# Kernel optimization log

Measured on AMD Instinct MI355X. Metric: run time of the kernel, lower is better.

The kernel has to match this reference:

```python
import jax, jax.numpy as jnp
import numpy as np

NUM_EXPERTS = 8
TOP_K = 2
AUX_COEF = 0.01
B, S, D, H = 4, 2048, 1024, 684


def setup_inputs() -> dict:
    key = jax.random.key(0)
    ks = jax.random.split(key, 5)
    scale_d = 1.0 / np.sqrt(D)
    scale_h = 1.0 / np.sqrt(H)
    return {
        "x": jax.random.normal(ks[0], (B, S, D), dtype=jnp.float32),
        "router_w": jax.random.normal(ks[1], (NUM_EXPERTS, D), dtype=jnp.float32) * scale_d,
        "w1": jax.random.normal(ks[2], (NUM_EXPERTS, H, D), dtype=jnp.float32) * scale_d,
        "w2": jax.random.normal(ks[3], (NUM_EXPERTS, D, H), dtype=jnp.float32) * scale_h,
        "w3": jax.random.normal(ks[4], (NUM_EXPERTS, H, D), dtype=jnp.float32) * scale_d,
    }


def reference(x, router_w, w1, w2, w3):
    b, s, d = x.shape
    xf = x.reshape(-1, d)                                   # [T, d]
    probs = jax.nn.softmax(xf @ router_w.T, axis=-1)        # [T, E]
    topk_probs, topk_idx = jax.lax.top_k(probs, TOP_K)      # [T, k]

    # aux load-balancing loss (uses top-1 assignment density)
    density = jnp.mean(jax.nn.one_hot(topk_idx[:, 0], NUM_EXPERTS, dtype=xf.dtype), axis=0)
    aux_loss = AUX_COEF * jnp.sum(density * probs.mean(axis=0)) * NUM_EXPERTS

    # per-token per-expert combine weight (sums probs if an expert repeats across slots)
    combine = jnp.sum(jax.nn.one_hot(topk_idx, NUM_EXPERTS, dtype=xf.dtype)
                      * topk_probs[..., None], axis=1)      # [T, E]

    out = jnp.zeros_like(xf)
    for e in range(NUM_EXPERTS):  # fixed small expert loop
        h = jax.nn.silu(xf @ w1[e].T) * (xf @ w3[e].T)      # [T, H] SwiGLU
        out = out + combine[:, e:e + 1] * (h @ w2[e].T)     # weighted scatter-combine
    return out.reshape(b, s, d), aux_loss
```

## Files before the change

### kernel.cpp

```cpp
#include <hip/hip_runtime.h>
#include <hip/hip_bf16.h>

#define T_TOK 8192
#define DMODEL 1024
#define HDIM 684
#define HPAD 704
#define NEXP 8

typedef short  bf16x8  __attribute__((ext_vector_type(8)));
typedef float  f32x4   __attribute__((ext_vector_type(4)));

__device__ inline unsigned short f2bu(float f) {
    __hip_bfloat16 h = __float2bfloat16(f);
    return *reinterpret_cast<unsigned short*>(&h);
}

typedef const __attribute__((address_space(1))) unsigned int* gas_p;
typedef __attribute__((address_space(3))) unsigned int* las_p;
__device__ inline void ld_lds16(const unsigned short* g, unsigned short* l) {
    __builtin_amdgcn_global_load_lds((gas_p)g, (las_p)l, 16, 0, 0);
}


__global__ __launch_bounds__(256) void cvt_all(
    const float* __restrict__ w1, const float* __restrict__ w3, const float* __restrict__ w2,
    unsigned short* __restrict__ w1b, unsigned short* __restrict__ w3b,
    unsigned short* __restrict__ w2b, int n4, int n2)
{
    int i = blockIdx.x * 256 + threadIdx.x;
    if (i < 2 * n4) {
        const float* src; unsigned short* dst; int j;
        if (i < n4) { src = w1; dst = w1b; j = i; }
        else        { src = w3; dst = w3b; j = i - n4; }
        float4 v = ((const float4*)src)[j];
        ((ushort4*)dst)[j] = make_ushort4(f2bu(v.x), f2bu(v.y), f2bu(v.z), f2bu(v.w));
        return;
    }
    int j = i - 2 * n4;
    if (j >= n2) return;
    int row = j / 176;
    int col = (j - row * 176) * 4;
    ushort4 o = make_ushort4(0, 0, 0, 0);
    if (col < HDIM) {
        float4 v = *(const float4*)(w2 + (size_t)row * HDIM + col);
        o = make_ushort4(f2bu(v.x), f2bu(v.y), f2bu(v.z), f2bu(v.w));
    }
    *(ushort4*)(w2b + (size_t)row * HPAD + col) = o;
}

__global__ __launch_bounds__(256) void moe_router(
    const float* __restrict__ x, const float* __restrict__ rw,
    unsigned short* __restrict__ xb,
    float* __restrict__ blk_psum, int* __restrict__ blk_t1, int* __restrict__ blk_pc,
    int* __restrict__ topk_idx, float* __restrict__ topk_p)
{
    __shared__ float sp[4][NEXP];
    __shared__ int   si1[4], si2[4];

    int lane = threadIdx.x & 63;
    int w    = threadIdx.x >> 6;
    int t    = blockIdx.x * 4 + w;
    const float* xr = x + (size_t)t * DMODEL;
    unsigned short* xbr = xb + (size_t)t * DMODEL;

    float acc[NEXP];
#pragma unroll
    for (int e = 0; e < NEXP; ++e) acc[e] = 0.f;
#pragma unroll
    for (int j = 0; j < DMODEL / 64; ++j) {
        float xv = xr[j * 64 + lane];
        xbr[j * 64 + lane] = f2bu(xv);
#pragma unroll
        for (int e = 0; e < NEXP; ++e)
            acc[e] += xv * rw[e * DMODEL + j * 64 + lane];
    }
#pragma unroll
    for (int off = 32; off > 0; off >>= 1) {
#pragma unroll
        for (int e = 0; e < NEXP; ++e)
            acc[e] += __shfl_xor(acc[e], off, 64);
    }
    if (lane == 0) {
        float m = acc[0];
#pragma unroll
        for (int e = 1; e < NEXP; ++e) m = fmaxf(m, acc[e]);
        float p[NEXP]; float s = 0.f;
#pragma unroll
        for (int e = 0; e < NEXP; ++e) { p[e] = expf(acc[e] - m); s += p[e]; }
        float inv = 1.f / s;
#pragma unroll
        for (int e = 0; e < NEXP; ++e) p[e] *= inv;
        int i1 = 0;
#pragma unroll
        for (int e = 1; e < NEXP; ++e) if (p[e] > p[i1]) i1 = e;
        int i2 = (i1 == 0) ? 1 : 0;
#pragma unroll
        for (int e = 0; e < NEXP; ++e) if (e != i1 && p[e] > p[i2]) i2 = e;

        topk_idx[t * 2 + 0] = i1;  topk_idx[t * 2 + 1] = i2;
        topk_p[t * 2 + 0] = p[i1]; topk_p[t * 2 + 1] = p[i2];
#pragma unroll
        for (int e = 0; e < NEXP; ++e) sp[w][e] = p[e];
        si1[w] = i1; si2[w] = i2;
    }
    __syncthreads();
    if (threadIdx.x < NEXP) {
        int e = threadIdx.x;
        float ps = sp[0][e] + sp[1][e] + sp[2][e] + sp[3][e];
        int t1 = (si1[0] == e) + (si1[1] == e) + (si1[2] == e) + (si1[3] == e);
        int pc = t1 + (si2[0] == e) + (si2[1] == e) + (si2[2] == e) + (si2[3] == e);
        blk_psum[blockIdx.x * NEXP + e] = ps;
        blk_t1[blockIdx.x * NEXP + e]  = t1;
        blk_pc[blockIdx.x * NEXP + e]  = pc;
    }
}

__global__ __launch_bounds__(256) void moe_scan(
    const float* __restrict__ blk_psum, const int* __restrict__ blk_t1,
    const int* __restrict__ blk_pc,
    int* pair_count, int* offsets, int* cursor, float* aux_out)
{
    __shared__ float wp[4][NEXP];
    __shared__ int   wt[4][NEXP], wc[4][NEXP];
    __shared__ float tp[NEXP];
    __shared__ int   tt1[NEXP], tpc[NEXP];

    int tid = threadIdx.x;
    int lane = tid & 63, w = tid >> 6;
    float lp[NEXP]; int lt[NEXP], lc[NEXP];
#pragma unroll
    for (int e = 0; e < NEXP; ++e) { lp[e] = 0.f; lt[e] = 0; lc[e] = 0; }
    for (int b = tid; b < 2048; b += 256)
#pragma unroll
        for (int e = 0; e < NEXP; ++e) {
            lp[e] += blk_psum[b * NEXP + e];
            lt[e] += blk_t1[b * NEXP + e];
            lc[e] += blk_pc[b * NEXP + e];
        }
#pragma unroll
    for (int off = 32; off > 0; off >>= 1) {
#pragma unroll
        for (int e = 0; e < NEXP; ++e) {
            lp[e] += __shfl_xor(lp[e], off, 64);
            lt[e] += __shfl_xor(lt[e], off, 64);
            lc[e] += __shfl_xor(lc[e], off, 64);
        }
    }
    if (lane == 0) {
#pragma unroll
        for (int e = 0; e < NEXP; ++e) { wp[w][e] = lp[e]; wt[w][e] = lt[e]; wc[w][e] = lc[e]; }
    }
    __syncthreads();
    if (tid < NEXP) {
        int e = tid;
        float s = wp[0][e] + wp[1][e] + wp[2][e] + wp[3][e];
        int t1 = wt[0][e] + wt[1][e] + wt[2][e] + wt[3][e];
        int pc = wc[0][e] + wc[1][e] + wc[2][e] + wc[3][e];
        tp[e] = s; tt1[e] = t1; tpc[e] = pc;
        pair_count[e] = pc;
    }
    __syncthreads();
    if (tid == 0) {
        int run = 0;
        for (int e = 0; e < NEXP; ++e) { offsets[e] = run; cursor[e] = run; run += tpc[e]; }
        float s = 0.f;
        for (int e = 0; e < NEXP; ++e)
            s += ((float)tt1[e] / (float)T_TOK) * (tp[e] / (float)T_TOK);
        aux_out[0] = 0.01f * s * (float)NEXP;
    }
}

__global__ __launch_bounds__(256) void moe_scatter(
    const int* __restrict__ topk_idx, const float* __restrict__ topk_p,
    int* cursor, int* __restrict__ pair_token, float* __restrict__ pair_prob)
{
    __shared__ int lcnt[NEXP], gbase[NEXP];
    int tid = threadIdx.x;
    if (tid < NEXP) lcnt[tid] = 0;
    __syncthreads();
    int t = blockIdx.x * 256 + tid;
    int e0 = topk_idx[t * 2 + 0], e1 = topk_idx[t * 2 + 1];
    int p0 = atomicAdd(&lcnt[e0], 1);
    int p1 = atomicAdd(&lcnt[e1], 1);
    __syncthreads();
    if (tid < NEXP) gbase[tid] = atomicAdd(&cursor[tid], lcnt[tid]);
    __syncthreads();
    int q0 = gbase[e0] + p0, q1 = gbase[e1] + p1;
    pair_token[q0] = t; pair_prob[q0] = topk_p[t * 2 + 0];
    pair_token[q1] = t; pair_prob[q1] = topk_p[t * 2 + 1];
}


__global__ __launch_bounds__(512, 4) void moe_ffn1(
    const unsigned short* __restrict__ xb, const unsigned short* __restrict__ w1b,
    const unsigned short* __restrict__ w3b,
    const int* __restrict__ pair_count, const int* __restrict__ offsets,
    const int* __restrict__ pair_token,
    unsigned short* __restrict__ h)
{
    int e   = blockIdx.z;
    int cnt = pair_count[e];
    int m0  = blockIdx.y * 128;
    if (m0 >= cnt) return;
    int base = offsets[e];
    int n0   = blockIdx.x * 128;

    __shared__ unsigned short aT[3 * 4096];
    __shared__ unsigned short b1T[3 * 4096];
    __shared__ unsigned short b3T[3 * 4096];

    int tid  = threadIdx.x;
    int lane = tid & 63, wave = tid >> 6;
    int wm = wave >> 1, wn = wave & 1;

    int srow = lane >> 2;
    int ksg  = (lane & 3) ^ ((lane >> 3) & 3);
    int arow = m0 + wave * 16 + srow; if (arow >= cnt) arow = cnt - 1;
    const unsigned short* ap  = xb + (size_t)pair_token[base + arow] * DMODEL + ksg * 8;
    int brow = n0 + wave * 16 + srow; if (brow > HDIM - 1) brow = HDIM - 1;
    const unsigned short* b1p = w1b + ((size_t)e * HDIM + brow) * DMODEL + ksg * 8;
    const unsigned short* b3p = w3b + ((size_t)e * HDIM + brow) * DMODEL + ksg * 8;
    unsigned short* sA  = aT  + wave * 512;
    unsigned short* sB1 = b1T + wave * 512;
    unsigned short* sB3 = b3T + wave * 512;

    f32x4 acc1[2][4], acc3[2][4];
#pragma unroll
    for (int i = 0; i < 2; ++i)
#pragma unroll
        for (int j = 0; j < 4; ++j) { acc1[i][j] = (f32x4)(0.f); acc3[i][j] = (f32x4)(0.f); }

    int fr  = lane & 15;
    int sz8 = ((lane >> 4) ^ ((fr >> 1) & 3)) * 8;

    ld_lds16(ap,        sA);
    ld_lds16(b1p,       sB1);
    ld_lds16(b3p,       sB3);
    ld_lds16(ap  + 32,  sA  + 4096);
    ld_lds16(b1p + 32,  sB1 + 4096);
    ld_lds16(b3p + 32,  sB3 + 4096);

    const int NIT = DMODEL / 32;
    for (int it = 0; it < NIT; ++it) {
        int buf = it % 3;
        if (it + 1 < NIT) asm volatile("s_waitcnt vmcnt(3)" ::: "memory");
        else              asm volatile("s_waitcnt vmcnt(0)" ::: "memory");
        __builtin_amdgcn_s_barrier();
        asm volatile("" ::: "memory");
        if (it + 2 < NIT) {
            int nb = (it + 2) % 3;
            int nk = (it + 2) * 32;
            ld_lds16(ap  + nk, sA  + nb * 4096);
            ld_lds16(b1p + nk, sB1 + nb * 4096);
            ld_lds16(b3p + nk, sB3 + nb * 4096);
        }
        const unsigned short* cA  = aT  + buf * 4096;
        const unsigned short* cB1 = b1T + buf * 4096;
        const unsigned short* cB3 = b3T + buf * 4096;

        bf16x8 aF[2];
#pragma unroll
        for (int i = 0; i < 2; ++i)
            aF[i] = *(const bf16x8*)&cA[(wm * 32 + i * 16 + fr) * 32 + sz8];
        __builtin_amdgcn_s_setprio(1);
#pragma unroll
        for (int j = 0; j < 4; ++j) {
            int row = (wn * 64 + j * 16 + fr) * 32 + sz8;
            bf16x8 b1F = *(const bf16x8*)&cB1[row];
            bf16x8 b3F = *(const bf16x8*)&cB3[row];
#pragma unroll
            for (int i = 0; i < 2; ++i) {
                acc1[i][j] = __builtin_amdgcn_mfma_f32_16x16x32_bf16(aF[i], b1F, acc1[i][j], 0, 0, 0);
                acc3[i][j] = __builtin_amdgcn_mfma_f32_16x16x32_bf16(aF[i], b3F, acc3[i][j], 0, 0, 0);
            }
        }
        __builtin_amdgcn_s_setprio(0);
    }

    int cbase = n0 + wn * 64 + fr;
    int rbase = m0 + wm * 32 + (lane >> 4) * 4;
#pragma unroll
    for (int i = 0; i < 2; ++i) {
#pragma unroll
        for (int r = 0; r < 4; ++r) {
            int gr = rbase + i * 16 + r;
            if (gr >= cnt) continue;
            unsigned short* hrow = h + (size_t)(base + gr) * HPAD;
#pragma unroll
            for (int j = 0; j < 4; ++j) {
                int col = cbase + j * 16;
                if (col >= HPAD) continue;
                float v1 = acc1[i][j][r];
                float hv = (col < HDIM) ? (v1 / (1.f + expf(-v1))) * acc3[i][j][r] : 0.f;
                hrow[col] = f2bu(hv);
            }
        }
    }
}

__global__ __launch_bounds__(512, 4) void moe_ffn2(
    const unsigned short* __restrict__ h, const unsigned short* __restrict__ w2b,
    const int* __restrict__ pair_count, const int* __restrict__ offsets,
    const int* __restrict__ pair_token, const float* __restrict__ pair_prob,
    float* __restrict__ out)
{
    int e   = blockIdx.z;
    int cnt = pair_count[e];
    int m0  = blockIdx.y * 128;
    if (m0 >= cnt) return;
    int base = offsets[e];
    int n0   = blockIdx.x * 256;

    __shared__ unsigned short aT[3 * 4096];
    __shared__ unsigned short bT[3 * 8192];

    int tid  = threadIdx.x;
    int lane = tid & 63, wave = tid >> 6;
    int wm = wave >> 1, wn = wave & 1;

    int srow = lane >> 2;
    int ksg  = (lane & 3) ^ ((lane >> 3) & 3);
    int arow = m0 + wave * 16 + srow; if (arow >= cnt) arow = cnt - 1;
    const unsigned short* ap = h + (size_t)(base + arow) * HPAD + ksg * 8;
    const unsigned short* bp = w2b + ((size_t)e * DMODEL + n0 + wave * 32 + srow) * HPAD + ksg * 8;
    unsigned short* sA = aT + wave * 512;
    unsigned short* sB = bT + wave * 1024;

    f32x4 acc[2][8];
#pragma unroll
    for (int i = 0; i < 2; ++i)
#pragma unroll
        for (int j = 0; j < 8; ++j) acc[i][j] = (f32x4)(0.f);

    int fr  = lane & 15;
    int sz8 = ((lane >> 4) ^ ((fr >> 1) & 3)) * 8;

    ld_lds16(ap,                  sA);
    ld_lds16(bp,                  sB);
    ld_lds16(bp + 16 * HPAD,      sB + 512);
    ld_lds16(ap + 32,             sA + 4096);
    ld_lds16(bp + 32,             sB + 8192);
    ld_lds16(bp + 16 * HPAD + 32, sB + 8192 + 512);

    const int NIT = HPAD / 32;
    for (int it = 0; it < NIT; ++it) {
        int buf = it % 3;
        if (it + 1 < NIT) asm volatile("s_waitcnt vmcnt(3)" ::: "memory");
        else              asm volatile("s_waitcnt vmcnt(0)" ::: "memory");
        __builtin_amdgcn_s_barrier();
        asm volatile("" ::: "memory");
        if (it + 2 < NIT) {
            int nb = (it + 2) % 3;
            int nk = (it + 2) * 32;
            ld_lds16(ap + nk,             sA + nb * 4096);
            ld_lds16(bp + nk,             sB + nb * 8192);
            ld_lds16(bp + 16 * HPAD + nk, sB + nb * 8192 + 512);
        }
        const unsigned short* cA = aT + buf * 4096;
        const unsigned short* cB = bT + buf * 8192;

        bf16x8 aF[2];
#pragma unroll
        for (int i = 0; i < 2; ++i)
            aF[i] = *(const bf16x8*)&cA[(wm * 32 + i * 16 + fr) * 32 + sz8];
        __builtin_amdgcn_s_setprio(1);
#pragma unroll
        for (int j = 0; j < 8; ++j) {
            bf16x8 bF = *(const bf16x8*)&cB[(wn * 128 + j * 16 + fr) * 32 + sz8];
#pragma unroll
            for (int i = 0; i < 2; ++i)
                acc[i][j] = __builtin_amdgcn_mfma_f32_16x16x32_bf16(aF[i], bF, acc[i][j], 0, 0, 0);
        }
        __builtin_amdgcn_s_setprio(0);
    }

    int cbase = n0 + wn * 128 + fr;
    int rbase = m0 + wm * 32 + (lane >> 4) * 4;
#pragma unroll
    for (int i = 0; i < 2; ++i) {
#pragma unroll
        for (int r = 0; r < 4; ++r) {
            int gr = rbase + i * 16 + r;
            if (gr >= cnt) continue;
            int gp = base + gr;
            float pw = pair_prob[gp];
            float* orow = out + (size_t)pair_token[gp] * DMODEL;
#pragma unroll
            for (int j = 0; j < 8; ++j)
                atomicAdd(&orow[cbase + j * 16], pw * acc[i][j][r]);
        }
    }
}

extern "C" void kernel_launch(void* const* d_in, const int* in_sizes, int n_in,
                              void* d_out, int out_size, void* d_ws, size_t ws_size,
                              hipStream_t stream)
{
    const float* x  = (const float*)d_in[0];
    const float* rw = (const float*)d_in[1];
    const float* w1 = (const float*)d_in[2];
    const float* w2 = (const float*)d_in[3];
    const float* w3 = (const float*)d_in[4];
    float* out = (float*)d_out;

    char* ws = (char*)d_ws;
    int*   pair_count = (int*)(ws + 0);
    int*   offsets    = (int*)(ws + 32);
    int*   cursor     = (int*)(ws + 64);
    float* blk_psum   = (float*)(ws + 256);
    int*   blk_t1     = (int*)(ws + 65792);
    int*   blk_pc     = (int*)(ws + 131328);
    int*   topk_idx   = (int*)(ws + 196864);
    float* topk_p     = (float*)(ws + 262400);
    int*   pair_token = (int*)(ws + 327936);
    float* pair_prob  = (float*)(ws + 393472);
    unsigned short* xb  = (unsigned short*)(ws + 459264);
    unsigned short* w1b = (unsigned short*)(ws + 17236480);
    unsigned short* w3b = (unsigned short*)(ws + 28443136);
    unsigned short* w2b = (unsigned short*)(ws + 39649792);
    unsigned short* hbuf= (unsigned short*)(ws + 51184128);

    hipMemsetAsync(d_out, 0, (size_t)out_size * sizeof(float), stream);

    int n4 = NEXP * HDIM * DMODEL / 4;
    int n2 = NEXP * DMODEL * (HPAD / 4);
    cvt_all<<<(2 * n4 + n2 + 255) / 256, 256, 0, stream>>>(w1, w3, w2, w1b, w3b, w2b, n4, n2);

    moe_router <<<T_TOK / 4, 256, 0, stream>>>(x, rw, xb, blk_psum, blk_t1, blk_pc, topk_idx, topk_p);
    moe_scan   <<<1, 256, 0, stream>>>(blk_psum, blk_t1, blk_pc, pair_count, offsets, cursor,
                                       out + (size_t)T_TOK * DMODEL);
    moe_scatter<<<T_TOK / 256, 256, 0, stream>>>(topk_idx, topk_p, cursor, pair_token, pair_prob);

    moe_ffn1<<<dim3(6, 64, 8), 512, 0, stream>>>(xb, w1b, w3b, pair_count, offsets, pair_token, hbuf);
    moe_ffn2<<<dim3(4, 64, 8), 512, 0, stream>>>(hbuf, w2b, pair_count, offsets, pair_token, pair_prob, out);
}
```

Before: 326.3 us.

## Replace atomic scatter-add in FFN2 with per-pair stores and a combine pass

FFN2 now writes each weighted pair output to a dense per-pair buffer instead of doing float atomicAdds into the token output, and a new combine kernel sums each token's two pair rows using positions recorded by the scatter kernel. This removes the output memset and the atomic contention, at the cost of an extra 64MB write and read. The FFN2 N-tile is also halved from 256 to 128, doubling the grid. The new path only runs if the workspace is large enough; otherwise it falls back to atomics.

```diff
diff --git a/kernel.cpp b/kernel.cpp
--- a/kernel.cpp
+++ b/kernel.cpp
@@ -21,6 +21,9 @@
     __builtin_amdgcn_global_load_lds((gas_p)g, (las_p)l, 16, 0, 0);
 }
 
+#define POS_OFF    74252800ull
+#define PAIRS_OFF  74318336ull
+#define WS_NEED   141427200ull
 
 __global__ __launch_bounds__(256) void cvt_all(
     const float* __restrict__ w1, const float* __restrict__ w3, const float* __restrict__ w2,
@@ -172,7 +175,8 @@
 
 __global__ __launch_bounds__(256) void moe_scatter(
     const int* __restrict__ topk_idx, const float* __restrict__ topk_p,
-    int* cursor, int* __restrict__ pair_token, float* __restrict__ pair_prob)
+    int* cursor, int* __restrict__ pair_token, float* __restrict__ pair_prob,
+    int* __restrict__ pos)
 {
     __shared__ int lcnt[NEXP], gbase[NEXP];
     int tid = threadIdx.x;
@@ -188,6 +192,7 @@
     int q0 = gbase[e0] + p0, q1 = gbase[e1] + p1;
     pair_token[q0] = t; pair_prob[q0] = topk_p[t * 2 + 0];
     pair_token[q1] = t; pair_prob[q1] = topk_p[t * 2 + 1];
+    pos[t * 2 + 0] = q0; pos[t * 2 + 1] = q1;
 }
 
 
@@ -302,17 +307,17 @@
     const unsigned short* __restrict__ h, const unsigned short* __restrict__ w2b,
     const int* __restrict__ pair_count, const int* __restrict__ offsets,
     const int* __restrict__ pair_token, const float* __restrict__ pair_prob,
-    float* __restrict__ out)
+    float* __restrict__ pairs_out, float* __restrict__ out, int use_atomic)
 {
     int e   = blockIdx.z;
     int cnt = pair_count[e];
     int m0  = blockIdx.y * 128;
     if (m0 >= cnt) return;
     int base = offsets[e];
-    int n0   = blockIdx.x * 256;
+    int n0   = blockIdx.x * 128;
 
     __shared__ unsigned short aT[3 * 4096];
-    __shared__ unsigned short bT[3 * 8192];
+    __shared__ unsigned short bT[3 * 4096];
 
     int tid  = threadIdx.x;
     int lane = tid & 63, wave = tid >> 6;
@@ -322,42 +327,39 @@
     int ksg  = (lane & 3) ^ ((lane >> 3) & 3);
     int arow = m0 + wave * 16 + srow; if (arow >= cnt) arow = cnt - 1;
     const unsigned short* ap = h + (size_t)(base + arow) * HPAD + ksg * 8;
-    const unsigned short* bp = w2b + ((size_t)e * DMODEL + n0 + wave * 32 + srow) * HPAD + ksg * 8;
+    const unsigned short* bp = w2b + ((size_t)e * DMODEL + n0 + wave * 16 + srow) * HPAD + ksg * 8;
     unsigned short* sA = aT + wave * 512;
-    unsigned short* sB = bT + wave * 1024;
-
-    f32x4 acc[2][8];
+    unsigned short* sB = bT + wave * 512;
+
+    f32x4 acc[2][4];
 #pragma unroll
     for (int i = 0; i < 2; ++i)
 #pragma unroll
-        for (int j = 0; j < 8; ++j) acc[i][j] = (f32x4)(0.f);
+        for (int j = 0; j < 4; ++j) acc[i][j] = (f32x4)(0.f);
 
     int fr  = lane & 15;
     int sz8 = ((lane >> 4) ^ ((fr >> 1) & 3)) * 8;
 
-    ld_lds16(ap,                  sA);
-    ld_lds16(bp,                  sB);
-    ld_lds16(bp + 16 * HPAD,      sB + 512);
-    ld_lds16(ap + 32,             sA + 4096);
-    ld_lds16(bp + 32,             sB + 8192);
-    ld_lds16(bp + 16 * HPAD + 32, sB + 8192 + 512);
+    ld_lds16(ap,      sA);
+    ld_lds16(bp,      sB);
+    ld_lds16(ap + 32, sA + 4096);
+    ld_lds16(bp + 32, sB + 4096);
 
     const int NIT = HPAD / 32;
     for (int it = 0; it < NIT; ++it) {
         int buf = it % 3;
-        if (it + 1 < NIT) asm volatile("s_waitcnt vmcnt(3)" ::: "memory");
+        if (it + 1 < NIT) asm volatile("s_waitcnt vmcnt(2)" ::: "memory");
         else              asm volatile("s_waitcnt vmcnt(0)" ::: "memory");
         __builtin_amdgcn_s_barrier();
         asm volatile("" ::: "memory");
         if (it + 2 < NIT) {
             int nb = (it + 2) % 3;
             int nk = (it + 2) * 32;
-            ld_lds16(ap + nk,             sA + nb * 4096);
-            ld_lds16(bp + nk,             sB + nb * 8192);
-            ld_lds16(bp + 16 * HPAD + nk, sB + nb * 8192 + 512);
+            ld_lds16(ap + nk, sA + nb * 4096);
+            ld_lds16(bp + nk, sB + nb * 4096);
         }
         const unsigned short* cA = aT + buf * 4096;
-        const unsigned short* cB = bT + buf * 8192;
+        const unsigned short* cB = bT + buf * 4096;
 
         bf16x8 aF[2];
 #pragma unroll
@@ -365,8 +367,8 @@
             aF[i] = *(const bf16x8*)&cA[(wm * 32 + i * 16 + fr) * 32 + sz8];
         __builtin_amdgcn_s_setprio(1);
 #pragma unroll
-        for (int j = 0; j < 8; ++j) {
-            bf16x8 bF = *(const bf16x8*)&cB[(wn * 128 + j * 16 + fr) * 32 + sz8];
+        for (int j = 0; j < 4; ++j) {
+            bf16x8 bF = *(const bf16x8*)&cB[(wn * 64 + j * 16 + fr) * 32 + sz8];
 #pragma unroll
             for (int i = 0; i < 2; ++i)
                 acc[i][j] = __builtin_amdgcn_mfma_f32_16x16x32_bf16(aF[i], bF, acc[i][j], 0, 0, 0);
@@ -374,7 +376,7 @@
         __builtin_amdgcn_s_setprio(0);
     }
 
-    int cbase = n0 + wn * 128 + fr;
+    int cbase = n0 + wn * 64 + fr;
     int rbase = m0 + wm * 32 + (lane >> 4) * 4;
 #pragma unroll
     for (int i = 0; i < 2; ++i) {
@@ -384,12 +386,33 @@
             if (gr >= cnt) continue;
             int gp = base + gr;
             float pw = pair_prob[gp];
-            float* orow = out + (size_t)pair_token[gp] * DMODEL;
-#pragma unroll
-            for (int j = 0; j < 8; ++j)
-                atomicAdd(&orow[cbase + j * 16], pw * acc[i][j][r]);
-        }
-    }
+            if (!use_atomic) {
+                float* prow = pairs_out + (size_t)gp * DMODEL;
+#pragma unroll
+                for (int j = 0; j < 4; ++j)
+                    prow[cbase + j * 16] = pw * acc[i][j][r];
+            } else {
+                float* orow = out + (size_t)pair_token[gp] * DMODEL;
+#pragma unroll
+                for (int j = 0; j < 4; ++j)
+                    atomicAdd(&orow[cbase + j * 16], pw * acc[i][j][r]);
+            }
+        }
+    }
+}
+
+__global__ __launch_bounds__(256) void moe_combine(
+    const float* __restrict__ pairs_out, const int* __restrict__ pos,
+    float* __restrict__ out)
+{
+    int t = blockIdx.x;
+    int c = threadIdx.x;
+    int q0 = pos[t * 2 + 0], q1 = pos[t * 2 + 1];
+    float4 a = ((const float4*)(pairs_out + (size_t)q0 * DMODEL))[c];
+    float4 b = ((const float4*)(pairs_out + (size_t)q1 * DMODEL))[c];
+    float4 o;
+    o.x = a.x + b.x; o.y = a.y + b.y; o.z = a.z + b.z; o.w = a.w + b.w;
+    ((float4*)(out + (size_t)t * DMODEL))[c] = o;
 }
 
 extern "C" void kernel_launch(void* const* d_in, const int* in_sizes, int n_in,
@@ -419,8 +442,12 @@
     unsigned short* w3b = (unsigned short*)(ws + 28443136);
     unsigned short* w2b = (unsigned short*)(ws + 39649792);
     unsigned short* hbuf= (unsigned short*)(ws + 51184128);
-
-    hipMemsetAsync(d_out, 0, (size_t)out_size * sizeof(float), stream);
+    int*   pos        = (int*)(ws + POS_OFF);
+    float* pairs_out  = (float*)(ws + PAIRS_OFF);
+
+    int two_pass = (ws_size >= WS_NEED) ? 1 : 0;
+    if (!two_pass)
+        hipMemsetAsync(d_out, 0, (size_t)out_size * sizeof(float), stream);
 
     int n4 = NEXP * HDIM * DMODEL / 4;
     int n2 = NEXP * DMODEL * (HPAD / 4);
@@ -429,8 +456,11 @@
     moe_router <<<T_TOK / 4, 256, 0, stream>>>(x, rw, xb, blk_psum, blk_t1, blk_pc, topk_idx, topk_p);
     moe_scan   <<<1, 256, 0, stream>>>(blk_psum, blk_t1, blk_pc, pair_count, offsets, cursor,
                                        out + (size_t)T_TOK * DMODEL);
-    moe_scatter<<<T_TOK / 256, 256, 0, stream>>>(topk_idx, topk_p, cursor, pair_token, pair_prob);
+    moe_scatter<<<T_TOK / 256, 256, 0, stream>>>(topk_idx, topk_p, cursor, pair_token, pair_prob, pos);
 
     moe_ffn1<<<dim3(6, 64, 8), 512, 0, stream>>>(xb, w1b, w3b, pair_count, offsets, pair_token, hbuf);
-    moe_ffn2<<<dim3(4, 64, 8), 512, 0, stream>>>(hbuf, w2b, pair_count, offsets, pair_token, pair_prob, out);
-}
+    moe_ffn2<<<dim3(8, 64, 8), 512, 0, stream>>>(hbuf, w2b, pair_count, offsets, pair_token, pair_prob,
+                                                 pairs_out, out, two_pass ? 0 : 1);
+    if (two_pass)
+        moe_combine<<<T_TOK, 256, 0, stream>>>(pairs_out, pos, out);
+}
```

Measured after the change: 302.9 us. 7.2% less time.
